# Kernel tuning notes

Measured on AMD Instinct MI355X. Metric: run time of the kernel, lower is better.

Reference implementation:

```python
import jax, jax.numpy as jnp
import numpy as np

DILATIONS = [1, 2, 4]


def _lstm_cell(x, h, c, W_ih, W_hh, b_ih, b_hh):
    # PyTorch LSTMCell: gates in i, f, g, o order
    gates = x @ W_ih.T + b_ih + h @ W_hh.T + b_hh
    i, f, g, o = jnp.split(gates, 4, axis=-1)
    c_new = jax.nn.sigmoid(f) * c + jax.nn.sigmoid(i) * jnp.tanh(g)
    h_new = jax.nn.sigmoid(o) * jnp.tanh(c_new)
    return h_new, c_new


def _drnn_forward(x, params):
    B, T, _ = x.shape
    H = params[0][1].shape[1]
    L = len(params)
    # static per-(t, layer) update mask from dilations
    masks = jnp.asarray(
        np.array([[t % d == 0 for d in DILATIONS] for t in range(T)], dtype=bool)
    )  # [T, L]

    hs0 = tuple(jnp.zeros((B, H), x.dtype) for _ in range(L))
    cs0 = tuple(jnp.zeros((B, H), x.dtype) for _ in range(L))

    def step(carry, inp):
        hs, cs = carry
        x_t, m = inp  # x_t: [B, F], m: [L] bool
        hs = list(hs)
        cs = list(cs)
        for l, (Wi, Wh, bi, bh) in enumerate(params):
            inp_l = x_t if l == 0 else hs[l - 1]
            h_new, c_new = _lstm_cell(inp_l, hs[l], cs[l], Wi, Wh, bi, bh)
            hs[l] = jnp.where(m[l], h_new, hs[l])
            cs[l] = jnp.where(m[l], c_new, cs[l])
        return (tuple(hs), tuple(cs)), hs[-1]

    _, ys = jax.lax.scan(step, (hs0, cs0), (jnp.swapaxes(x, 0, 1), masks))
    return jnp.swapaxes(ys, 0, 1)  # [B, T, H]


def setup_inputs() -> dict:
    key = jax.random.key(0)
    ks = jax.random.split(key, 16)
    B, T, F, H = 128, 1024, 128, 256
    k = 1.0 / np.sqrt(H)  # torch LSTMCell init scale

    def u(kk, shape):
        return jax.random.uniform(kk, shape, jnp.float32, -k, k)

    inp = {"x": jax.random.normal(ks[0], (B, T, F), jnp.float32)}
    in_sizes = [F, H, H]
    ki = 1
    for l in range(3):
        inp[f"W_ih{l}"] = u(ks[ki], (4 * H, in_sizes[l])); ki += 1
        inp[f"W_hh{l}"] = u(ks[ki], (4 * H, H)); ki += 1
        inp[f"b_ih{l}"] = u(ks[ki], (4 * H,)); ki += 1
        inp[f"b_hh{l}"] = u(ks[ki], (4 * H,)); ki += 1
    return inp


def reference(x, W_ih0, W_hh0, b_ih0, b_hh0,
              W_ih1, W_hh1, b_ih1, b_hh1,
              W_ih2, W_hh2, b_ih2, b_hh2):
    params = [
        (W_ih0, W_hh0, b_ih0, b_hh0),
        (W_ih1, W_hh1, b_ih1, b_hh1),
        (W_ih2, W_hh2, b_ih2, b_hh2),
    ]
    return _drnn_forward(x, params)
```

## Files before the change

kernel.cpp:

```cpp
#include <hip/hip_runtime.h>
#include <hip/hip_fp16.h>
#include <stdint.h>
#include <stddef.h>


typedef _Float16 f16;
typedef _Float16 v2h __attribute__((ext_vector_type(2)));
typedef _Float16 v8h __attribute__((ext_vector_type(8)));
typedef __fp16 h2_raw __attribute__((ext_vector_type(2)));
typedef __fp16 h8_raw __attribute__((ext_vector_type(8)));
typedef float v4f __attribute__((ext_vector_type(4)));
typedef unsigned long long u64;

#define DEVINL static __device__ __forceinline__

DEVINL float sigm(float x) { return 1.0f / (1.0f + __expf(-x)); }
DEVINL float tanh_(float x) {
  x = fminf(fmaxf(x, -15.0f), 15.0f);
  float e = __expf(-2.0f * x);
  return (1.0f - e) / (1.0f + e);
}
DEVINL v2h pack2(float a, float b) {
  return __builtin_bit_cast(v2h, __builtin_amdgcn_cvt_pkrtz(a, b));
}
DEVINL v4f mfma_16x16x32(v8h a, v8h b, v4f c) {
  return __builtin_amdgcn_mfma_f32_16x16x32_f16(__builtin_bit_cast(h8_raw, a),
                                                __builtin_bit_cast(h8_raw, b), c,
                                                0, 0, 0);
}

DEVINL void wg_barrier() {
  __builtin_amdgcn_sched_barrier(0);
  asm volatile("s_waitcnt lgkmcnt(0)" ::: "memory");
  __builtin_amdgcn_s_barrier();
  asm volatile("" ::: "memory");
  __builtin_amdgcn_sched_barrier(0);
}


__global__ void k_cvt_x(const float2* __restrict__ src, v2h* __restrict__ dst, int n2) {
  int i = blockIdx.x * blockDim.x + threadIdx.x;
  int st = gridDim.x * blockDim.x;
  for (; i < n2; i += st) {
    float2 v = src[i];
    dst[i] = pack2(v.x, v.y);
  }
}

__global__ void k_prep_w(const float* __restrict__ wih0, const float* __restrict__ whh0,
                         const float* __restrict__ wih1, const float* __restrict__ whh1,
                         const float* __restrict__ wih2, const float* __restrict__ whh2,
                         const float* __restrict__ bi0, const float* __restrict__ bh0,
                         const float* __restrict__ bi1, const float* __restrict__ bh1,
                         const float* __restrict__ bi2, const float* __restrict__ bh2,
                         f16* wih0f, f16* whh0f, f16* wih1f, f16* whh1f,
                         f16* wih2f, f16* whh2f,
                         float* bias0, float* bias1, float* bias2) {
  int i = blockIdx.x * blockDim.x + threadIdx.x;
  if (i < 131072) wih0f[i] = (f16)wih0[i];
  whh0f[i] = (f16)whh0[i];
  wih1f[i] = (f16)wih1[i];
  whh1f[i] = (f16)whh1[i];
  wih2f[i] = (f16)wih2[i];
  whh2f[i] = (f16)whh2[i];
  if (i < 1024) {
    bias0[i] = bi0[i] + bh0[i];
    bias1[i] = bi1[i] + bh1[i];
    bias2[i] = bi2[i] + bh2[i];
  }
}


template <int K>
__launch_bounds__(256)
__global__ void k_gemm(const f16* __restrict__ A, int Tb, int t0,
                       const f16* __restrict__ W, const float* __restrict__ bias,
                       f16* __restrict__ G) {
  constexpr int LDK = K + 8;
  __shared__ f16 As[64 * LDK];
  int b = blockIdx.x >> 2, tb = blockIdx.x & 3;
  const f16* Ablk = A + ((size_t)b * Tb + t0 + tb * 64) * K;
  int tid = threadIdx.x;

  constexpr int NV = 64 * K / 8;
  const uint4* src = (const uint4*)Ablk;
  for (int i = tid; i < NV; i += 256) {
    int e = i * 8;
    int r = e / K, c0 = e % K;
    *(uint4*)&As[r * LDK + c0] = src[i];
  }
  __syncthreads();

  int wave = tid >> 6, lane = tid & 63;
  int lm = lane & 15, lk = (lane >> 4) * 8;

  v8h af[K / 32];
#pragma unroll
  for (int kc = 0; kc < K / 32; ++kc)
    af[kc] = *(const v8h*)&As[(wave * 16 + lm) * LDK + kc * 32 + lk];

  size_t grow0 = (size_t)b * 256 + tb * 64 + wave * 16;
  for (int nt = 0; nt < 64; ++nt) {
    v4f acc = {0.0f, 0.0f, 0.0f, 0.0f};
    const f16* Wrow = W + (size_t)(nt * 16 + lm) * K + lk;
#pragma unroll
    for (int kc = 0; kc < K / 32; ++kc) {
      v8h bf = *(const v8h*)(Wrow + kc * 32);
      acc = mfma_16x16x32(af[kc], bf, acc);
    }
    float bv = bias[nt * 16 + lm];
#pragma unroll
    for (int r = 0; r < 4; ++r) {
      int m = (lane >> 4) * 4 + r;
      G[(grow0 + m) * 1024 + nt * 16 + lm] = (f16)(acc[r] + bv);
    }
  }
}


template <int LAYER>
__launch_bounds__(256)
__global__ void k_rec(const f16* __restrict__ G,
                      const f16* __restrict__ Whh,
                      int t0, int steps,
                      f16* __restrict__ Hout, float* __restrict__ y,
                      float* __restrict__ hstate, float* __restrict__ cstate,
                      u64* hxw) {
  int blk = blockIdx.x;
  int g = blk & 15, sub = blk >> 4;
  int d0 = sub * 16;
  int tid = threadIdx.x;
  int lane = tid & 63, wv = tid >> 6;
  int q = wv;
  int arow = lane & 15, s4 = lane >> 4;

  bool is_cell = (lane < 16);
  int bl = 2 * wv + (lane >> 3);
  int wp = lane & 7;
  int b = g * 8 + bl;

  int pbl = tid >> 5;
  int pwd = (tid & 31) * 4;

  __shared__ __align__(16) f16 hbuf[16][256];
  __shared__ float gq[4][8][18];

  v8h wf[8];
  {
    const v8h* wrow = (const v8h*)&Whh[(size_t)(q * 256 + d0 + arow) * 256];
#pragma unroll
    for (int kt = 0; kt < 8; ++kt) wf[kt] = wrow[kt * 4 + s4];
#pragma unroll
    for (int i = 0; i < 8; ++i)
      asm volatile("" : "+v"(wf[i]));
  }

  char* fillp = (char*)hbuf + pbl * 512 + (((tid & 31) ^ (pbl & 7)) * 16);
  char* fillz = (char*)hbuf + (8 + pbl) * 512 + (((tid & 31) ^ (pbl & 7)) * 16);

  float c0 = 0.f, c1 = 0.f, h0 = 0.f, h1 = 0.f;
  {
    uint4 z = {0u, 0u, 0u, 0u};
    *(uint4*)fillz = z;
    if (t0 == 0) {
      *(uint4*)fillp = z;
    } else {
      int bq = g * 8 + pbl;
      const float4* hs = (const float4*)&hstate[(size_t)bq * 256 + 2 * pwd];
      float4 u = hs[0], v = hs[1];
      uint4 pk;
      pk.x = __builtin_bit_cast(uint32_t, pack2(u.x, u.y));
      pk.y = __builtin_bit_cast(uint32_t, pack2(u.z, u.w));
      pk.z = __builtin_bit_cast(uint32_t, pack2(v.x, v.y));
      pk.w = __builtin_bit_cast(uint32_t, pack2(v.z, v.w));
      *(uint4*)fillp = pk;
      if (is_cell) {
        float2 cc = *(const float2*)&cstate[(size_t)b * 256 + d0 + 2 * wp];
        c0 = cc.x; c1 = cc.y;
      }
    }
  }
  __syncthreads();

  u64* hx_g = hxw + (size_t)g * 2048;
  u64* pubp = hx_g + (size_t)bl * 128 + (d0 >> 1) + wp;
  const u64* pollp = hx_g + (size_t)pbl * 128 + pwd;

  const f16* Gc = G + (size_t)b * 262144 + d0 + 2 * wp;
  uint32_t gv[4] = {0, 0, 0, 0}, gn[4] = {0, 0, 0, 0};
  if (is_cell) {
#pragma unroll
    for (int j = 0; j < 4; ++j) gv[j] = *(const uint32_t*)&Gc[j * 256];
  }

  for (int s = 0; s < steps; ++s) {
    int t = t0 + s;
    int pp = (t + 1) & 1;

    v4f acc0 = {0.f, 0.f, 0.f, 0.f}, acc1 = {0.f, 0.f, 0.f, 0.f};
#pragma unroll
    for (int kt = 0; kt < 8; kt += 2) {
      v8h a0 = *(const v8h*)((const char*)hbuf + arow * 512 +
                             (((kt * 4 + s4) ^ (arow & 7)) * 16));
      acc0 = mfma_16x16x32(a0, wf[kt], acc0);
      v8h a1 = *(const v8h*)((const char*)hbuf + arow * 512 +
                             ((((kt + 1) * 4 + s4) ^ (arow & 7)) * 16));
      acc1 = mfma_16x16x32(a1, wf[kt + 1], acc1);
    }
    if (lane < 32) {
      int r0 = s4 * 4;
#pragma unroll
      for (int r = 0; r < 4; ++r) gq[q][r0 + r][arow] = acc0[r] + acc1[r];
    }
    if (is_cell && s + 1 < steps) {
#pragma unroll
      for (int j = 0; j < 4; ++j)
        gn[j] = *(const uint32_t*)&Gc[(size_t)(s + 1) * 1024 + j * 256];
    }
    wg_barrier();

    if (is_cell) {
      float2 zi = *(const float2*)&gq[0][bl][2 * wp];
      float2 zf = *(const float2*)&gq[1][bl][2 * wp];
      float2 zg = *(const float2*)&gq[2][bl][2 * wp];
      float2 zo = *(const float2*)&gq[3][bl][2 * wp];
      v2h G0 = __builtin_bit_cast(v2h, gv[0]);
      v2h G1 = __builtin_bit_cast(v2h, gv[1]);
      v2h G2 = __builtin_bit_cast(v2h, gv[2]);
      v2h G3 = __builtin_bit_cast(v2h, gv[3]);
      float i0 = sigm(zi.x + (float)G0[0]), i1 = sigm(zi.y + (float)G0[1]);
      float f0 = sigm(zf.x + (float)G1[0]), f1 = sigm(zf.y + (float)G1[1]);
      float g0 = tanh_(zg.x + (float)G2[0]), g1 = tanh_(zg.y + (float)G2[1]);
      float o0 = sigm(zo.x + (float)G3[0]), o1 = sigm(zo.y + (float)G3[1]);
      c0 = f0 * c0 + i0 * g0;
      c1 = f1 * c1 + i1 * g1;
      h0 = o0 * tanh_(c0);
      h1 = o1 * tanh_(c1);

      uint32_t hp = __builtin_bit_cast(uint32_t, pack2(h0, h1));
      __hip_atomic_store(pubp + (size_t)pp * 1024,
                         ((u64)(uint32_t)(t + 1) << 32) | (u64)hp,
                         __ATOMIC_RELAXED, __HIP_MEMORY_SCOPE_AGENT);

      if (LAYER == 0) {
        if ((t & 1) == 0) {
          v2h hr; hr[0] = (f16)h0; hr[1] = (f16)h1;
          *(uint32_t*)&Hout[((size_t)b * 512 + (t >> 1)) * 256 + d0 + 2 * wp] =
              __builtin_bit_cast(uint32_t, hr);
        }
      } else if (LAYER == 1) {
        if ((t & 1) == 0) {
          v2h hr; hr[0] = (f16)h0; hr[1] = (f16)h1;
          *(uint32_t*)&Hout[((size_t)b * 256 + (t >> 1)) * 256 + d0 + 2 * wp] =
              __builtin_bit_cast(uint32_t, hr);
        }
      } else {
        size_t base = ((size_t)b * 1024 + (size_t)t * 4) * 256 + d0 + 2 * wp;
        float2 hv; hv.x = h0; hv.y = h1;
        *(float2*)&y[base] = hv;
        *(float2*)&y[base + 256] = hv;
        *(float2*)&y[base + 512] = hv;
        *(float2*)&y[base + 768] = hv;
      }
    }

    if (s + 1 < steps) {
      const u64* pb = pollp + (size_t)pp * 1024;
      int tau = t + 1;
      u64 w0, w1, w2, w3;
      for (;;) {
        w0 = __hip_atomic_load(pb + 0, __ATOMIC_RELAXED, __HIP_MEMORY_SCOPE_AGENT);
        w1 = __hip_atomic_load(pb + 1, __ATOMIC_RELAXED, __HIP_MEMORY_SCOPE_AGENT);
        w2 = __hip_atomic_load(pb + 2, __ATOMIC_RELAXED, __HIP_MEMORY_SCOPE_AGENT);
        w3 = __hip_atomic_load(pb + 3, __ATOMIC_RELAXED, __HIP_MEMORY_SCOPE_AGENT);
        if ((int)(w0 >> 32) >= tau && (int)(w1 >> 32) >= tau &&
            (int)(w2 >> 32) >= tau && (int)(w3 >> 32) >= tau)
          break;
      }
      uint4 pk;
      pk.x = (uint32_t)w0; pk.y = (uint32_t)w1;
      pk.z = (uint32_t)w2; pk.w = (uint32_t)w3;
      *(uint4*)fillp = pk;
    }
    wg_barrier();

    if (is_cell) {
#pragma unroll
      for (int j = 0; j < 4; ++j) gv[j] = gn[j];
    }
  }

  if (is_cell) {
    size_t sb = (size_t)b * 256 + d0 + 2 * wp;
    float2 hv; hv.x = h0; hv.y = h1;
    float2 cv; cv.x = c0; cv.y = c1;
    *(float2*)&hstate[sb] = hv;
    *(float2*)&cstate[sb] = cv;
  }
}


extern "C" void kernel_launch(void* const* d_in, const int* in_sizes, int n_in,
                              void* d_out, int out_size, void* d_ws, size_t ws_size,
                              hipStream_t stream) {
  const float* x = (const float*)d_in[0];
  const float* wih[3] = {(const float*)d_in[1], (const float*)d_in[5], (const float*)d_in[9]};
  const float* whh[3] = {(const float*)d_in[2], (const float*)d_in[6], (const float*)d_in[10]};
  const float* bi[3] = {(const float*)d_in[3], (const float*)d_in[7], (const float*)d_in[11]};
  const float* bh[3] = {(const float*)d_in[4], (const float*)d_in[8], (const float*)d_in[12]};
  float* y = (float*)d_out;

  char* p = (char*)d_ws;
  f16* Xf = (f16*)p;        p += (size_t)16777216 * 2;
  f16* Wih0f = (f16*)p;     p += (size_t)131072 * 2;
  f16* Whh0f = (f16*)p;     p += (size_t)262144 * 2;
  f16* Wih1f = (f16*)p;     p += (size_t)262144 * 2;
  f16* Whh1f = (f16*)p;     p += (size_t)262144 * 2;
  f16* Wih2f = (f16*)p;     p += (size_t)262144 * 2;
  f16* Whh2f = (f16*)p;     p += (size_t)262144 * 2;
  float* bias0 = (float*)p; p += 4096;
  float* bias1 = (float*)p; p += 4096;
  float* bias2 = (float*)p; p += 4096;
  f16* Gbuf = (f16*)p;      p += (size_t)32768 * 1024 * 2;
  f16* H0e = (f16*)p;       p += (size_t)128 * 512 * 256 * 2;
  f16* H1q = (f16*)p;       p += (size_t)128 * 256 * 256 * 2;
  float* hstate = (float*)p; p += (size_t)128 * 256 * 4;
  float* cstate = (float*)p; p += (size_t)128 * 256 * 4;
  u64* hxw0 = (u64*)p;      p += (size_t)16 * 2 * 1024 * 8;
  u64* hxw1 = (u64*)p;      p += (size_t)16 * 2 * 1024 * 8;
  u64* hxw2 = (u64*)p;      p += (size_t)16 * 2 * 1024 * 8;

  k_cvt_x<<<4096, 256, 0, stream>>>((const float2*)x, (v2h*)Xf, 8388608);
  k_prep_w<<<1024, 256, 0, stream>>>(wih[0], whh[0], wih[1], whh[1], wih[2], whh[2],
                                     bi[0], bh[0], bi[1], bh[1], bi[2], bh[2],
                                     Wih0f, Whh0f, Wih1f, Whh1f, Wih2f, Whh2f,
                                     bias0, bias1, bias2);

  for (int c = 0; c < 4; ++c) {
    k_gemm<128><<<512, 256, 0, stream>>>(Xf, 1024, c * 256, Wih0f, bias0, Gbuf);
    k_rec<0><<<256, 256, 0, stream>>>(Gbuf, Whh0f, c * 256, 256, H0e, nullptr,
                                      hstate, cstate, hxw0);
  }
  for (int c = 0; c < 2; ++c) {
    k_gemm<256><<<512, 256, 0, stream>>>(H0e, 512, c * 256, Wih1f, bias1, Gbuf);
    k_rec<1><<<256, 256, 0, stream>>>(Gbuf, Whh1f, c * 256, 256, H1q, nullptr,
                                      hstate, cstate, hxw1);
  }
  k_gemm<256><<<512, 256, 0, stream>>>(H1q, 256, 0, Wih2f, bias2, Gbuf);
  k_rec<2><<<256, 256, 0, stream>>>(Gbuf, Whh2f, 0, 256, nullptr, y,
                                    hstate, cstate, hxw2);
}
```

Before: 4.679 ms.

## Specialize waves: cell wave, G-prefetch wave via LDS ring, dedicated poll waves

Reworks the recurrent kernel's per-step schedule by giving each wavefront a role. Wave 0 computes all 64 cell outputs, wave 1 prefetches G three steps ahead through registers into a double-buffered LDS slot, and waves 2-3 spin on the global hx exchange, each thread filling 16 halves. The step loop is unrolled by four to rotate the prefetch registers. The aim is to hide G load latency and spread polling and cell work across waves, at the cost of extra LDS traffic and an assumption that steps is a multiple of four.

```diff
diff --git a/kernel.cpp b/kernel.cpp
--- a/kernel.cpp
+++ b/kernel.cpp
@@ -134,16 +134,17 @@
   int q = wv;
   int arow = lane & 15, s4 = lane >> 4;
 
-  bool is_cell = (lane < 16);
-  int bl = 2 * wv + (lane >> 3);
-  int wp = lane & 7;
-  int b = g * 8 + bl;
-
-  int pbl = tid >> 5;
-  int pwd = (tid & 31) * 4;
+  int bl0 = lane >> 3, wp = lane & 7;
+  int b0 = g * 8 + bl0;
+
+  int p128 = tid - 128;
+  int pbl = (p128 >> 4) & 7, subp = p128 & 15;
+
+  int bl1 = lane >> 3, qg = (lane & 7) >> 1, h8 = lane & 1;
 
   __shared__ __align__(16) f16 hbuf[16][256];
   __shared__ float gq[4][8][18];
+  __shared__ __align__(16) f16 Gl[2][8 * 72];
 
   v8h wf[8];
   {
@@ -151,147 +152,191 @@
 #pragma unroll
     for (int kt = 0; kt < 8; ++kt) wf[kt] = wrow[kt * 4 + s4];
 #pragma unroll
-    for (int i = 0; i < 8; ++i)
-      asm volatile("" : "+v"(wf[i]));
-  }
-
-  char* fillp = (char*)hbuf + pbl * 512 + (((tid & 31) ^ (pbl & 7)) * 16);
-  char* fillz = (char*)hbuf + (8 + pbl) * 512 + (((tid & 31) ^ (pbl & 7)) * 16);
+    for (int i = 0; i < 8; ++i) asm volatile("" : "+v"(wf[i]));
+  }
 
   float c0 = 0.f, c1 = 0.f, h0 = 0.f, h1 = 0.f;
   {
     uint4 z = {0u, 0u, 0u, 0u};
-    *(uint4*)fillz = z;
+    *(uint4*)((char*)hbuf + 4096 + tid * 16) = z;
     if (t0 == 0) {
-      *(uint4*)fillp = z;
+      *(uint4*)((char*)hbuf + tid * 16) = z;
     } else {
-      int bq = g * 8 + pbl;
-      const float4* hs = (const float4*)&hstate[(size_t)bq * 256 + 2 * pwd];
-      float4 u = hs[0], v = hs[1];
-      uint4 pk;
-      pk.x = __builtin_bit_cast(uint32_t, pack2(u.x, u.y));
-      pk.y = __builtin_bit_cast(uint32_t, pack2(u.z, u.w));
-      pk.z = __builtin_bit_cast(uint32_t, pack2(v.x, v.y));
-      pk.w = __builtin_bit_cast(uint32_t, pack2(v.z, v.w));
-      *(uint4*)fillp = pk;
-      if (is_cell) {
-        float2 cc = *(const float2*)&cstate[(size_t)b * 256 + d0 + 2 * wp];
+      if (wv >= 2) {
+        const float4* hs =
+            (const float4*)&hstate[(size_t)(g * 8 + pbl) * 256 + subp * 16];
+        float4 a = hs[0], bq = hs[1], cc = hs[2], dd = hs[3];
+        uint4 lo, hi;
+        lo.x = __builtin_bit_cast(uint32_t, pack2(a.x, a.y));
+        lo.y = __builtin_bit_cast(uint32_t, pack2(a.z, a.w));
+        lo.z = __builtin_bit_cast(uint32_t, pack2(bq.x, bq.y));
+        lo.w = __builtin_bit_cast(uint32_t, pack2(bq.z, bq.w));
+        hi.x = __builtin_bit_cast(uint32_t, pack2(cc.x, cc.y));
+        hi.y = __builtin_bit_cast(uint32_t, pack2(cc.z, cc.w));
+        hi.z = __builtin_bit_cast(uint32_t, pack2(dd.x, dd.y));
+        hi.w = __builtin_bit_cast(uint32_t, pack2(dd.z, dd.w));
+        int c0i = (2 * subp) ^ (pbl & 7), c1i = (2 * subp + 1) ^ (pbl & 7);
+        *(uint4*)((char*)hbuf + pbl * 512 + c0i * 16) = lo;
+        *(uint4*)((char*)hbuf + pbl * 512 + c1i * 16) = hi;
+      }
+      if (wv == 0) {
+        float2 cc = *(const float2*)&cstate[(size_t)b0 * 256 + d0 + 2 * wp];
         c0 = cc.x; c1 = cc.y;
+        float2 hh = *(const float2*)&hstate[(size_t)b0 * 256 + d0 + 2 * wp];
+        h0 = hh.x; h1 = hh.y;
       }
     }
   }
+
+  u64* hx_g = hxw + (size_t)g * 2048;
+  u64* pubp = hx_g + (size_t)bl0 * 128 + sub * 8 + wp;
+  const u64* pollp = hx_g + (size_t)pbl * 128 + subp * 8;
+
+  const f16* Gw = G + (size_t)(g * 8 + bl1) * 262144 + qg * 256 + d0 + h8 * 8;
+  char* GlW = (char*)Gl + bl1 * 144 + qg * 32 + h8 * 16;
+  uint4 g0r, g1r, g2r, g3r;
+  if (wv == 1) {
+    g0r = *(const uint4*)(Gw);
+    g1r = *(const uint4*)(Gw + 1024);
+    g2r = *(const uint4*)(Gw + 2048);
+    g3r = *(const uint4*)(Gw + 3072);
+    *(uint4*)(GlW) = g0r;
+  }
   __syncthreads();
-
-  u64* hx_g = hxw + (size_t)g * 2048;
-  u64* pubp = hx_g + (size_t)bl * 128 + (d0 >> 1) + wp;
-  const u64* pollp = hx_g + (size_t)pbl * 128 + pwd;
-
-  const f16* Gc = G + (size_t)b * 262144 + d0 + 2 * wp;
-  uint32_t gv[4] = {0, 0, 0, 0}, gn[4] = {0, 0, 0, 0};
-  if (is_cell) {
-#pragma unroll
-    for (int j = 0; j < 4; ++j) gv[j] = *(const uint32_t*)&Gc[j * 256];
-  }
-
-  for (int s = 0; s < steps; ++s) {
-    int t = t0 + s;
-    int pp = (t + 1) & 1;
-
-    v4f acc0 = {0.f, 0.f, 0.f, 0.f}, acc1 = {0.f, 0.f, 0.f, 0.f};
-#pragma unroll
-    for (int kt = 0; kt < 8; kt += 2) {
-      v8h a0 = *(const v8h*)((const char*)hbuf + arow * 512 +
-                             (((kt * 4 + s4) ^ (arow & 7)) * 16));
-      acc0 = mfma_16x16x32(a0, wf[kt], acc0);
-      v8h a1 = *(const v8h*)((const char*)hbuf + arow * 512 +
-                             ((((kt + 1) * 4 + s4) ^ (arow & 7)) * 16));
-      acc1 = mfma_16x16x32(a1, wf[kt + 1], acc1);
-    }
-    if (lane < 32) {
-      int r0 = s4 * 4;
-#pragma unroll
-      for (int r = 0; r < 4; ++r) gq[q][r0 + r][arow] = acc0[r] + acc1[r];
-    }
-    if (is_cell && s + 1 < steps) {
-#pragma unroll
-      for (int j = 0; j < 4; ++j)
-        gn[j] = *(const uint32_t*)&Gc[(size_t)(s + 1) * 1024 + j * 256];
-    }
-    wg_barrier();
-
-    if (is_cell) {
-      float2 zi = *(const float2*)&gq[0][bl][2 * wp];
-      float2 zf = *(const float2*)&gq[1][bl][2 * wp];
-      float2 zg = *(const float2*)&gq[2][bl][2 * wp];
-      float2 zo = *(const float2*)&gq[3][bl][2 * wp];
-      v2h G0 = __builtin_bit_cast(v2h, gv[0]);
-      v2h G1 = __builtin_bit_cast(v2h, gv[1]);
-      v2h G2 = __builtin_bit_cast(v2h, gv[2]);
-      v2h G3 = __builtin_bit_cast(v2h, gv[3]);
-      float i0 = sigm(zi.x + (float)G0[0]), i1 = sigm(zi.y + (float)G0[1]);
-      float f0 = sigm(zf.x + (float)G1[0]), f1 = sigm(zf.y + (float)G1[1]);
-      float g0 = tanh_(zg.x + (float)G2[0]), g1 = tanh_(zg.y + (float)G2[1]);
-      float o0 = sigm(zo.x + (float)G3[0]), o1 = sigm(zo.y + (float)G3[1]);
-      c0 = f0 * c0 + i0 * g0;
-      c1 = f1 * c1 + i1 * g1;
-      h0 = o0 * tanh_(c0);
-      h1 = o1 * tanh_(c1);
-
-      uint32_t hp = __builtin_bit_cast(uint32_t, pack2(h0, h1));
-      __hip_atomic_store(pubp + (size_t)pp * 1024,
-                         ((u64)(uint32_t)(t + 1) << 32) | (u64)hp,
-                         __ATOMIC_RELAXED, __HIP_MEMORY_SCOPE_AGENT);
-
-      if (LAYER == 0) {
-        if ((t & 1) == 0) {
-          v2h hr; hr[0] = (f16)h0; hr[1] = (f16)h1;
-          *(uint32_t*)&Hout[((size_t)b * 512 + (t >> 1)) * 256 + d0 + 2 * wp] =
-              __builtin_bit_cast(uint32_t, hr);
-        }
-      } else if (LAYER == 1) {
-        if ((t & 1) == 0) {
-          v2h hr; hr[0] = (f16)h0; hr[1] = (f16)h1;
-          *(uint32_t*)&Hout[((size_t)b * 256 + (t >> 1)) * 256 + d0 + 2 * wp] =
-              __builtin_bit_cast(uint32_t, hr);
-        }
-      } else {
-        size_t base = ((size_t)b * 1024 + (size_t)t * 4) * 256 + d0 + 2 * wp;
-        float2 hv; hv.x = h0; hv.y = h1;
-        *(float2*)&y[base] = hv;
-        *(float2*)&y[base + 256] = hv;
-        *(float2*)&y[base + 512] = hv;
-        *(float2*)&y[base + 768] = hv;
-      }
-    }
-
-    if (s + 1 < steps) {
-      const u64* pb = pollp + (size_t)pp * 1024;
-      int tau = t + 1;
-      u64 w0, w1, w2, w3;
-      for (;;) {
-        w0 = __hip_atomic_load(pb + 0, __ATOMIC_RELAXED, __HIP_MEMORY_SCOPE_AGENT);
-        w1 = __hip_atomic_load(pb + 1, __ATOMIC_RELAXED, __HIP_MEMORY_SCOPE_AGENT);
-        w2 = __hip_atomic_load(pb + 2, __ATOMIC_RELAXED, __HIP_MEMORY_SCOPE_AGENT);
-        w3 = __hip_atomic_load(pb + 3, __ATOMIC_RELAXED, __HIP_MEMORY_SCOPE_AGENT);
-        if ((int)(w0 >> 32) >= tau && (int)(w1 >> 32) >= tau &&
-            (int)(w2 >> 32) >= tau && (int)(w3 >> 32) >= tau)
-          break;
-      }
-      uint4 pk;
-      pk.x = (uint32_t)w0; pk.y = (uint32_t)w1;
-      pk.z = (uint32_t)w2; pk.w = (uint32_t)w3;
-      *(uint4*)fillp = pk;
-    }
-    wg_barrier();
-
-    if (is_cell) {
-#pragma unroll
-      for (int j = 0; j < 4; ++j) gv[j] = gn[j];
-    }
-  }
-
-  if (is_cell) {
-    size_t sb = (size_t)b * 256 + d0 + 2 * wp;
+  if (wv == 1) g0r = *(const uint4*)(Gw + 4096);
+
+  const char* gq0 = (const char*)gq;
+  const char* Glb = (const char*)Gl;
+
+#define CELL_AND_PUBLISH(J)                                                    \
+  {                                                                            \
+    float2 zi = *(const float2*)(gq0 + ((0 * 8 + bl0) * 18 + 2 * wp) * 4);     \
+    float2 zf = *(const float2*)(gq0 + ((1 * 8 + bl0) * 18 + 2 * wp) * 4);     \
+    float2 zg = *(const float2*)(gq0 + ((2 * 8 + bl0) * 18 + 2 * wp) * 4);     \
+    float2 zo = *(const float2*)(gq0 + ((3 * 8 + bl0) * 18 + 2 * wp) * 4);     \
+    const char* glr = Glb + ((J) & 1) * 1152 + bl0 * 144 + wp * 4;             \
+    v2h G0 = *(const v2h*)(glr);                                               \
+    v2h G1 = *(const v2h*)(glr + 32);                                          \
+    v2h G2 = *(const v2h*)(glr + 64);                                          \
+    v2h G3 = *(const v2h*)(glr + 96);                                          \
+    float i0 = sigm(zi.x + (float)G0[0]), i1 = sigm(zi.y + (float)G0[1]);      \
+    float f0 = sigm(zf.x + (float)G1[0]), f1 = sigm(zf.y + (float)G1[1]);      \
+    float gg0 = tanh_(zg.x + (float)G2[0]), gg1 = tanh_(zg.y + (float)G2[1]);  \
+    float o0 = sigm(zo.x + (float)G3[0]), o1 = sigm(zo.y + (float)G3[1]);      \
+    c0 = f0 * c0 + i0 * gg0;                                                   \
+    c1 = f1 * c1 + i1 * gg1;                                                   \
+    h0 = o0 * tanh_(c0);                                                       \
+    h1 = o1 * tanh_(c1);                                                       \
+    uint32_t hp = __builtin_bit_cast(uint32_t, pack2(h0, h1));                 \
+    __hip_atomic_store(pubp + (size_t)pp * 1024,                               \
+                       ((u64)(uint32_t)(t + 1) << 32) | (u64)hp,               \
+                       __ATOMIC_RELAXED, __HIP_MEMORY_SCOPE_AGENT);            \
+    if (LAYER == 0) {                                                          \
+      if ((t & 1) == 0) {                                                      \
+        v2h hr; hr[0] = (f16)h0; hr[1] = (f16)h1;                              \
+        *(uint32_t*)&Hout[((size_t)b0 * 512 + (t >> 1)) * 256 + d0 + 2 * wp] = \
+            __builtin_bit_cast(uint32_t, hr);                                  \
+      }                                                                        \
+    } else if (LAYER == 1) {                                                   \
+      if ((t & 1) == 0) {                                                      \
+        v2h hr; hr[0] = (f16)h0; hr[1] = (f16)h1;                              \
+        *(uint32_t*)&Hout[((size_t)b0 * 256 + (t >> 1)) * 256 + d0 + 2 * wp] = \
+            __builtin_bit_cast(uint32_t, hr);                                  \
+      }                                                                        \
+    } else {                                                                   \
+      size_t base = ((size_t)b0 * 1024 + (size_t)t * 4) * 256 + d0 + 2 * wp;   \
+      float2 hv; hv.x = h0; hv.y = h1;                                         \
+      *(float2*)&y[base] = hv;                                                 \
+      *(float2*)&y[base + 256] = hv;                                           \
+      *(float2*)&y[base + 512] = hv;                                           \
+      *(float2*)&y[base + 768] = hv;                                           \
+    }                                                                          \
+  }
+
+#define STEP(J, GWR, GLD)                                                      \
+  {                                                                            \
+    const int t = t0 + s + (J);                                                \
+    const int pp = (t + 1) & 1;                                                \
+                       \
+    v4f acc0 = {0.f, 0.f, 0.f, 0.f}, acc1 = {0.f, 0.f, 0.f, 0.f};              \
+    _Pragma("unroll") for (int kt = 0; kt < 8; kt += 2) {                      \
+      v8h a0 = *(const v8h*)((const char*)hbuf + arow * 512 +                  \
+                             (((kt * 4 + s4) ^ (arow & 7)) * 16));             \
+      acc0 = mfma_16x16x32(a0, wf[kt], acc0);                                  \
+      v8h a1 = *(const v8h*)((const char*)hbuf + arow * 512 +                  \
+                             ((((kt + 1) * 4 + s4) ^ (arow & 7)) * 16));       \
+      acc1 = mfma_16x16x32(a1, wf[kt + 1], acc1);                              \
+    }                                                                          \
+    if (lane < 32) {                                                           \
+      int r0 = s4 * 4;                                                         \
+      _Pragma("unroll") for (int r = 0; r < 4; ++r)                            \
+        gq[q][r0 + r][arow] = acc0[r] + acc1[r];                               \
+    }                                                                          \
+    if (wv == 1) {                                                             \
+      if (s + (J) + 1 < steps)                                                 \
+        *(uint4*)(GlW + (((J) + 1) & 1) * 1152) = GWR;                         \
+      if (s + (J) + 4 < steps)                                                 \
+        GLD = *(const uint4*)(Gw + ((size_t)(s + (J) + 4) << 10));             \
+    }                                                                          \
+    wg_barrier();                                                    \
+                                                      \
+    if (wv == 0) {                                                             \
+      CELL_AND_PUBLISH(J)                                                      \
+    } else if (wv >= 2) {                                                      \
+      if (s + (J) + 1 < steps) {                                               \
+        const u64* pb = pollp + (size_t)pp * 1024;                             \
+        int tau = t + 1;                                                       \
+        u64 w0 = __hip_atomic_load(pb, __ATOMIC_RELAXED,                       \
+                                   __HIP_MEMORY_SCOPE_AGENT);                  \
+        while ((int)(w0 >> 32) < tau)                                          \
+          w0 = __hip_atomic_load(pb, __ATOMIC_RELAXED,                         \
+                                 __HIP_MEMORY_SCOPE_AGENT);                    \
+        u64 w1, w2, w3, w4, w5, w6, w7;                                        \
+        for (;;) {                                                             \
+          w1 = __hip_atomic_load(pb + 1, __ATOMIC_RELAXED,                     \
+                                 __HIP_MEMORY_SCOPE_AGENT);                    \
+          w2 = __hip_atomic_load(pb + 2, __ATOMIC_RELAXED,                     \
+                                 __HIP_MEMORY_SCOPE_AGENT);                    \
+          w3 = __hip_atomic_load(pb + 3, __ATOMIC_RELAXED,                     \
+                                 __HIP_MEMORY_SCOPE_AGENT);                    \
+          w4 = __hip_atomic_load(pb + 4, __ATOMIC_RELAXED,                     \
+                                 __HIP_MEMORY_SCOPE_AGENT);                    \
+          w5 = __hip_atomic_load(pb + 5, __ATOMIC_RELAXED,                     \
+                                 __HIP_MEMORY_SCOPE_AGENT);                    \
+          w6 = __hip_atomic_load(pb + 6, __ATOMIC_RELAXED,                     \
+                                 __HIP_MEMORY_SCOPE_AGENT);                    \
+          w7 = __hip_atomic_load(pb + 7, __ATOMIC_RELAXED,                     \
+                                 __HIP_MEMORY_SCOPE_AGENT);                    \
+          if ((int)(w1 >> 32) >= tau && (int)(w2 >> 32) >= tau &&              \
+              (int)(w3 >> 32) >= tau && (int)(w4 >> 32) >= tau &&              \
+              (int)(w5 >> 32) >= tau && (int)(w6 >> 32) >= tau &&              \
+              (int)(w7 >> 32) >= tau)                                          \
+            break;                                                             \
+        }                                                                      \
+        uint4 lo, hi;                                                          \
+        lo.x = (uint32_t)w0; lo.y = (uint32_t)w1;                              \
+        lo.z = (uint32_t)w2; lo.w = (uint32_t)w3;                              \
+        hi.x = (uint32_t)w4; hi.y = (uint32_t)w5;                              \
+        hi.z = (uint32_t)w6; hi.w = (uint32_t)w7;                              \
+        int c0i = (2 * subp) ^ (pbl & 7), c1i = (2 * subp + 1) ^ (pbl & 7);    \
+        *(uint4*)((char*)hbuf + pbl * 512 + c0i * 16) = lo;                    \
+        *(uint4*)((char*)hbuf + pbl * 512 + c1i * 16) = hi;                    \
+      }                                                                        \
+    }                                                                          \
+    wg_barrier();                                                    \
+  }
+
+  for (int s = 0; s < steps; s += 4) {
+    STEP(0, g1r, g0r)
+    STEP(1, g2r, g1r)
+    STEP(2, g3r, g2r)
+    STEP(3, g0r, g3r)
+  }
+#undef STEP
+#undef CELL_AND_PUBLISH
+
+  if (wv == 0) {
+    size_t sb = (size_t)b0 * 256 + d0 + 2 * wp;
     float2 hv; hv.x = h0; hv.y = h1;
     float2 cv; cv.x = c0; cv.y = c1;
     *(float2*)&hstate[sb] = hv;
```

After: 5.206 ms. +11.3%, slower.
